# Optimization experiments

Measured on AMD Instinct MI355X. Metric: run time of the kernel, lower is better.

The kernel has to match this reference:

```python
import jax, jax.numpy as jnp
import numpy as np

N = 100000        # number of graph nodes
IN_DIM = 256      # input feature dim
OUT_DIM = 64      # output feature dim
X_NNZ = 1_600_000 # nnz of sparse feature matrix x (avg 16 per node)
A_NNZ = 3_200_000 # nnz of sparse adjacency (avg degree 32)
KEEP_PROB = 0.9   # 1 - dropout


def setup_inputs() -> dict:
    key = jax.random.key(0)
    ks = jax.random.split(key, 8)
    x_vals = jax.random.normal(ks[0], (X_NNZ,), dtype=jnp.float32)
    x_rows = jax.random.randint(ks[1], (X_NNZ,), 0, N, dtype=jnp.int32)
    x_cols = jax.random.randint(ks[2], (X_NNZ,), 0, IN_DIM, dtype=jnp.int32)
    adj_vals = jax.random.uniform(ks[3], (A_NNZ,), dtype=jnp.float32)
    adj_rows = jax.random.randint(ks[4], (A_NNZ,), 0, N, dtype=jnp.int32)
    adj_cols = jax.random.randint(ks[5], (A_NNZ,), 0, N, dtype=jnp.int32)
    # Glorot uniform init, as in weight_variable_glorot
    lim = float(np.sqrt(6.0 / (IN_DIM + OUT_DIM)))
    W = jax.random.uniform(ks[6], (IN_DIM, OUT_DIM), dtype=jnp.float32, minval=-lim, maxval=lim)
    # deterministic dropout retain mask (Bernoulli(keep_prob)), mirrors dropout_sparse
    keep_mask = jax.random.uniform(ks[7], (X_NNZ,)) < KEEP_PROB
    return {
        "x_vals": x_vals, "x_rows": x_rows, "x_cols": x_cols,
        "adj_vals": adj_vals, "adj_rows": adj_rows, "adj_cols": adj_cols,
        "W": W, "keep_mask": keep_mask,
    }


def reference(x_vals, x_rows, x_cols, adj_vals, adj_rows, adj_cols, W, keep_mask):
    # sparse dropout: retain + rescale by 1/keep_prob
    xv = jnp.where(keep_mask, x_vals, jnp.float32(0.0)) * jnp.float32(1.0 / KEEP_PROB)
    # spmm 1: h = x @ W  -> gather W rows by feature col index, scatter-add by node row
    h = jax.ops.segment_sum(xv[:, None] * W[x_cols], x_rows, num_segments=N)  # [N, OUT_DIM]
    # spmm 2: agg = adj @ h -> gather neighbor features, scatter-add by destination node
    agg = jax.ops.segment_sum(adj_vals[:, None] * h[adj_cols], adj_rows, num_segments=N)  # [N, OUT_DIM]
    return jax.nn.relu(agg)
```

## Files before the change

kernel.cpp:

```cpp
#include <hip/hip_runtime.h>
#include <hip/hip_bf16.h>

#define N_NODES 100000
#define IN_DIM 256
#define OUT_DIM 64
#define INV_KEEP 1.1111111111111112f

#define BROWS 256
#define NBUCKET ((N_NODES + BROWS - 1) / BROWS)
#define PBLK 256
#define A_CAP 9728
#define X_CAP 5120

__device__ __forceinline__ int   ldnt (const int* p)   { return __builtin_nontemporal_load(p); }
__device__ __forceinline__ float ldntf(const float* p) { return __builtin_nontemporal_load(p); }

__global__ __launch_bounds__(256) void hist_count_kernel(
    const int* __restrict__ xr, const int* __restrict__ keep,
    const int* __restrict__ ar,
    int* __restrict__ cnt_blk_x, int* __restrict__ cnt_blk_a,
    int x_nnz, int a_nnz)
{
    __shared__ int cnt[NBUCKET];
    const bool isA = blockIdx.x >= PBLK;
    const int ib = isA ? (int)blockIdx.x - PBLK : (int)blockIdx.x;
    const int nnz = isA ? a_nnz : x_nnz;
    const int chunk = (nnz + PBLK - 1) / PBLK;
    const int lo = ib * chunk, hi = min(lo + chunk, nnz);

    for (int k = threadIdx.x; k < NBUCKET; k += 256) cnt[k] = 0;
    __syncthreads();
    if (isA) {
        for (int e = lo + (int)threadIdx.x; e < hi; e += 256)
            atomicAdd(&cnt[ldnt(ar + e) >> 8], 1);
    } else {
        for (int e = lo + (int)threadIdx.x; e < hi; e += 256)
            if (ldnt(keep + e) != 0) atomicAdd(&cnt[ldnt(xr + e) >> 8], 1);
    }
    __syncthreads();
    int* dst = (isA ? cnt_blk_a : cnt_blk_x) + (size_t)ib * NBUCKET;
    for (int k = threadIdx.x; k < NBUCKET; k += 256) dst[k] = cnt[k];
}

__global__ __launch_bounds__(256) void colscan_kernel(
    int* __restrict__ cnt_blk_x, int* __restrict__ cnt_blk_a,
    int* __restrict__ btot_x, int* __restrict__ btot_a)
{
    const bool isA = blockIdx.x >= NBUCKET;
    const int k = isA ? (int)blockIdx.x - NBUCKET : (int)blockIdx.x;
    int* cb = isA ? cnt_blk_a : cnt_blk_x;
    __shared__ int sc[PBLK];
    const int t = threadIdx.x;
    int v = cb[(size_t)t * NBUCKET + k];
    sc[t] = v;
    __syncthreads();
    for (int off = 1; off < PBLK; off <<= 1) {
        int u = (t >= off) ? sc[t - off] : 0;
        __syncthreads();
        sc[t] += u;
        __syncthreads();
    }
    cb[(size_t)t * NBUCKET + k] = sc[t] - v;
    if (t == PBLK - 1) (isA ? btot_a : btot_x)[k] = sc[t];
}

__global__ __launch_bounds__(512) void bucket_scan_kernel(
    const int* __restrict__ btot_x, const int* __restrict__ btot_a,
    int* __restrict__ bstart_x, int* __restrict__ bstart_a)
{
    const int* c = blockIdx.x ? btot_a : btot_x;
    int* bs      = blockIdx.x ? bstart_a : bstart_x;
    __shared__ int sc[512];
    const int t = threadIdx.x;
    sc[t] = (t < NBUCKET) ? c[t] : 0;
    __syncthreads();
    for (int off = 1; off < 512; off <<= 1) {
        int u = (t >= off) ? sc[t - off] : 0;
        __syncthreads();
        sc[t] += u;
        __syncthreads();
    }
    if (t < NBUCKET) bs[t] = (t > 0) ? sc[t - 1] : 0;
    if (t == NBUCKET - 1) bs[NBUCKET] = sc[t];
}

__global__ __launch_bounds__(256) void partition_place_kernel(
    const float* __restrict__ xv, const int* __restrict__ xr,
    const int* __restrict__ xc, const int* __restrict__ keep,
    const float* __restrict__ av, const int* __restrict__ ar,
    const int* __restrict__ ac,
    const int* __restrict__ cnt_blk_x, const int* __restrict__ cnt_blk_a,
    const int* __restrict__ bstart_x, const int* __restrict__ bstart_a,
    float2* __restrict__ xs, float2* __restrict__ as, int x_nnz, int a_nnz)
{
    __shared__ int off_l[NBUCKET];
    const bool isA = blockIdx.x >= PBLK;
    const int ib = isA ? (int)blockIdx.x - PBLK : (int)blockIdx.x;
    const int nnz = isA ? a_nnz : x_nnz;
    const int chunk = (nnz + PBLK - 1) / PBLK;
    const int lo = ib * chunk, hi = min(lo + chunk, nnz);
    const int* cb = (isA ? cnt_blk_a : cnt_blk_x) + (size_t)ib * NBUCKET;
    const int* bs = isA ? bstart_a : bstart_x;
    float2* out   = isA ? as : xs;

    for (int k = threadIdx.x; k < NBUCKET; k += 256) off_l[k] = bs[k] + cb[k];
    __syncthreads();
    if (isA) {
        for (int e = lo + (int)threadIdx.x; e < hi; e += 256) {
            int r = ldnt(ar + e), c = ldnt(ac + e);
            float v = ldntf(av + e);
            int pos = atomicAdd(&off_l[r >> 8], 1);
            out[pos] = make_float2(v, __uint_as_float(((unsigned)c << 8) | (unsigned)(r & (BROWS - 1))));
        }
    } else {
        for (int e = lo + (int)threadIdx.x; e < hi; e += 256) {
            if (ldnt(keep + e) == 0) continue;
            int r = ldnt(xr + e), c = ldnt(xc + e);
            float v = ldntf(xv + e) * INV_KEEP;
            int pos = atomicAdd(&off_l[r >> 8], 1);
            out[pos] = make_float2(v, __uint_as_float(((unsigned)c << 8) | (unsigned)(r & (BROWS - 1))));
        }
    }
}

template <int CAP>
__global__ __launch_bounds__(256) void reorder_kernel(
    const int* __restrict__ bstart, float2* __restrict__ data,
    int* __restrict__ start)
{
    __shared__ float2 recs[CAP];
    __shared__ int rcnt[BROWS];
    __shared__ int sc[BROWS];
    __shared__ int curs[BROWS];
    const int b = blockIdx.x;
    const int brow0 = b * BROWS;
    const int rows_n = min(BROWS, N_NODES - brow0);
    const int base = bstart[b];
    int size = bstart[b + 1] - base;
    if (size > CAP) size = CAP;
    const int t = threadIdx.x;

    rcnt[t] = 0;
    __syncthreads();
    for (int i = t; i < size; i += 256) {
        float2 rec = data[base + i];
        recs[i] = rec;
        atomicAdd(&rcnt[__float_as_uint(rec.y) & (BROWS - 1)], 1);
    }
    __syncthreads();
    sc[t] = rcnt[t];
    __syncthreads();
    for (int off = 1; off < 256; off <<= 1) {
        int v = (t >= off) ? sc[t - off] : 0;
        __syncthreads();
        sc[t] += v;
        __syncthreads();
    }
    int excl = (t > 0) ? sc[t - 1] : 0;
    curs[t] = base + excl;
    if (t < rows_n) start[brow0 + t] = base + excl;
    if (brow0 + rows_n == N_NODES && t == rows_n - 1) start[N_NODES] = base + size;
    __syncthreads();
    for (int i = t; i < size; i += 256) {
        float2 rec = recs[i];
        unsigned u = __float_as_uint(rec.y);
        int pos = atomicAdd(&curs[u & (BROWS - 1)], 1);
        data[pos] = make_float2(rec.x, __int_as_float((int)(u >> 8)));
    }
}


__global__ __launch_bounds__(256) void spmm1_csr_kernel(
    const int* __restrict__ xs_start, const float2* __restrict__ xs,
    const float* __restrict__ W, __hip_bfloat16* __restrict__ h)
{
    const int wave = (int)((blockIdx.x * blockDim.x + threadIdx.x) >> 6);
    const int lane = threadIdx.x & 63;
    if (wave >= N_NODES) return;

    const int s = xs_start[wave];
    const int e = xs_start[wave + 1];
    float acc = 0.0f;
    int j = s;
    for (; j + 4 <= e; j += 4) {
        float2 p0 = xs[j + 0];
        float2 p1 = xs[j + 1];
        float2 p2 = xs[j + 2];
        float2 p3 = xs[j + 3];
        float g0 = W[__float_as_int(p0.y) * OUT_DIM + lane];
        float g1 = W[__float_as_int(p1.y) * OUT_DIM + lane];
        float g2 = W[__float_as_int(p2.y) * OUT_DIM + lane];
        float g3 = W[__float_as_int(p3.y) * OUT_DIM + lane];
        acc += p0.x * g0;
        acc += p1.x * g1;
        acc += p2.x * g2;
        acc += p3.x * g3;
    }
    for (; j < e; ++j) {
        float2 p = xs[j];
        acc += p.x * W[__float_as_int(p.y) * OUT_DIM + lane];
    }
    h[(size_t)wave * OUT_DIM + lane] = __float2bfloat16(acc);
}

__global__ __launch_bounds__(256) void spmm2_csr_kernel(
    const int* __restrict__ as_start, const float2* __restrict__ as,
    const __hip_bfloat16* __restrict__ h, float* __restrict__ out)
{
    const int wave = (int)((blockIdx.x * blockDim.x + threadIdx.x) >> 6);
    const int lane = threadIdx.x & 63;
    if (wave >= N_NODES) return;

    const int s = as_start[wave];
    const int e = as_start[wave + 1];
    float acc = 0.0f;
    int j = s;
    for (; j + 16 <= e; j += 16) {
        float2 q[16];
#pragma unroll
        for (int k = 0; k < 16; ++k) q[k] = as[j + k];
        float g[16];
#pragma unroll
        for (int k = 0; k < 16; ++k)
            g[k] = __bfloat162float(h[(size_t)__float_as_int(q[k].y) * OUT_DIM + lane]);
#pragma unroll
        for (int k = 0; k < 16; ++k) acc += q[k].x * g[k];
    }
    for (; j + 8 <= e; j += 8) {
        float2 q[8];
#pragma unroll
        for (int k = 0; k < 8; ++k) q[k] = as[j + k];
        float g[8];
#pragma unroll
        for (int k = 0; k < 8; ++k)
            g[k] = __bfloat162float(h[(size_t)__float_as_int(q[k].y) * OUT_DIM + lane]);
#pragma unroll
        for (int k = 0; k < 8; ++k) acc += q[k].x * g[k];
    }
    for (; j < e; ++j) {
        float2 p = as[j];
        acc += p.x * __bfloat162float(h[(size_t)__float_as_int(p.y) * OUT_DIM + lane]);
    }
    float r = acc > 0.0f ? acc : 0.0f;
    __builtin_nontemporal_store(r, &out[(size_t)wave * OUT_DIM + lane]);
}


__global__ __launch_bounds__(256) void spmm1_atomic_kernel(
    const float* __restrict__ x_vals, const int* __restrict__ x_rows,
    const int* __restrict__ x_cols, const int* __restrict__ keep,
    const float* __restrict__ W, float* __restrict__ h, int nnz)
{
    const int lane   = threadIdx.x & 63;
    const int group  = (int)((blockIdx.x * blockDim.x + threadIdx.x) >> 6);
    const int stride = (int)((gridDim.x * blockDim.x) >> 6);
    for (int e = group; e < nnz; e += stride) {
        float v = (keep[e] != 0) ? x_vals[e] * INV_KEEP : 0.0f;
        if (v != 0.0f)
            atomicAdd(&h[(size_t)x_rows[e] * OUT_DIM + lane],
                      v * W[x_cols[e] * OUT_DIM + lane]);
    }
}

__global__ __launch_bounds__(256) void spmm2_atomic_kernel(
    const float* __restrict__ adj_vals, const int* __restrict__ adj_rows,
    const int* __restrict__ adj_cols, const float* __restrict__ h,
    float* __restrict__ out, int nnz)
{
    const int lane   = threadIdx.x & 63;
    const int group  = (int)((blockIdx.x * blockDim.x + threadIdx.x) >> 6);
    const int stride = (int)((gridDim.x * blockDim.x) >> 6);
    for (int e = group; e < nnz; e += stride) {
        atomicAdd(&out[(size_t)adj_rows[e] * OUT_DIM + lane],
                  adj_vals[e] * h[(size_t)adj_cols[e] * OUT_DIM + lane]);
    }
}

__global__ __launch_bounds__(256) void relu_kernel(float* __restrict__ out, int n)
{
    int i = (int)(blockIdx.x * blockDim.x + threadIdx.x);
    if (i < n) {
        float v = out[i];
        out[i] = v > 0.0f ? v : 0.0f;
    }
}


extern "C" void kernel_launch(void* const* d_in, const int* in_sizes, int n_in,
                              void* d_out, int out_size, void* d_ws, size_t ws_size,
                              hipStream_t stream)
{
    const float* x_vals   = (const float*)d_in[0];
    const int*   x_rows   = (const int*)d_in[1];
    const int*   x_cols   = (const int*)d_in[2];
    const float* adj_vals = (const float*)d_in[3];
    const int*   adj_rows = (const int*)d_in[4];
    const int*   adj_cols = (const int*)d_in[5];
    const float* W        = (const float*)d_in[6];
    const int*   keep     = (const int*)d_in[7];

    const int x_nnz = in_sizes[0];
    const int a_nnz = in_sizes[3];

    float* out = (float*)d_out;

    char* ws = (char*)d_ws;
    size_t off = 0;
    float2* xs = (float2*)(ws + off);                 off += (size_t)x_nnz * 8;
    float2* as = (float2*)(ws + off);                 off += (size_t)a_nnz * 8;
    __hip_bfloat16* hb = (__hip_bfloat16*)(ws + off); off += (size_t)N_NODES * OUT_DIM * 2;
    int* x_start   = (int*)(ws + off);                off += (size_t)(N_NODES + 1) * 4;
    int* a_start   = (int*)(ws + off);                off += (size_t)(N_NODES + 1) * 4;
    int* cnt_blk_x = (int*)(ws + off);                off += (size_t)PBLK * NBUCKET * 4;
    int* cnt_blk_a = (int*)(ws + off);                off += (size_t)PBLK * NBUCKET * 4;
    int* btot_x    = (int*)(ws + off);                off += (size_t)NBUCKET * 4;
    int* btot_a    = (int*)(ws + off);                off += (size_t)NBUCKET * 4;
    int* bstart_x  = (int*)(ws + off);                off += (size_t)(NBUCKET + 1) * 4;
    int* bstart_a  = (int*)(ws + off);                off += (size_t)(NBUCKET + 1) * 4;
    const size_t needed = off;

    if (ws_size >= needed) {
        hist_count_kernel<<<2 * PBLK, 256, 0, stream>>>(
            x_rows, keep, adj_rows, cnt_blk_x, cnt_blk_a, x_nnz, a_nnz);

        colscan_kernel<<<2 * NBUCKET, 256, 0, stream>>>(
            cnt_blk_x, cnt_blk_a, btot_x, btot_a);

        bucket_scan_kernel<<<2, 512, 0, stream>>>(
            btot_x, btot_a, bstart_x, bstart_a);

        partition_place_kernel<<<2 * PBLK, 256, 0, stream>>>(
            x_vals, x_rows, x_cols, keep, adj_vals, adj_rows, adj_cols,
            cnt_blk_x, cnt_blk_a, bstart_x, bstart_a, xs, as, x_nnz, a_nnz);

        reorder_kernel<X_CAP><<<NBUCKET, 256, 0, stream>>>(bstart_x, xs, x_start);
        reorder_kernel<A_CAP><<<NBUCKET, 256, 0, stream>>>(bstart_a, as, a_start);

        const int blocks = (N_NODES * 64 + 255) / 256;
        spmm1_csr_kernel<<<blocks, 256, 0, stream>>>(x_start, xs, W, hb);
        spmm2_csr_kernel<<<blocks, 256, 0, stream>>>(a_start, as, hb, out);
    } else {
        float* hf = (float*)d_ws;
        hipMemsetAsync(hf, 0, (size_t)N_NODES * OUT_DIM * 4, stream);
        hipMemsetAsync(out, 0, (size_t)out_size * 4, stream);
        spmm1_atomic_kernel<<<4096, 256, 0, stream>>>(x_vals, x_rows, x_cols, keep, W, hf, x_nnz);
        spmm2_atomic_kernel<<<4096, 256, 0, stream>>>(adj_vals, adj_rows, adj_cols, hf, out, a_nnz);
        relu_kernel<<<(out_size + 255) / 256, 256, 0, stream>>>(out, out_size);
    }
}
```

Measured before the change: 301.4 us.

## Fuse x-bucket row reorder into spmm1, computing h directly from shared memory

The separate reorder pass for the feature matrix and the per-row CSR spmm1 kernel are merged into one kernel per 256-row bucket. It sorts the bucket's records by row into shared memory, then each of its 4 waves walks 64 rows and gathers W. This removes one global write and re-read of the x records, the x_start array and a launch. The cost is parallelism: spmm1 now runs on only about 391 blocks with 4 waves each, with serial row loops instead of one wave per row.

```diff
diff --git a/kernel.cpp b/kernel.cpp
--- a/kernel.cpp
+++ b/kernel.cpp
@@ -123,12 +123,80 @@
     }
 }
 
-template <int CAP>
-__global__ __launch_bounds__(256) void reorder_kernel(
+__global__ __launch_bounds__(256) void spmm1_fused_kernel(
+    const int* __restrict__ bstart, const float2* __restrict__ xs,
+    const float* __restrict__ W, __hip_bfloat16* __restrict__ h)
+{
+    __shared__ float2 recs[X_CAP];
+    __shared__ int rcnt[BROWS];
+    __shared__ int rofs[BROWS];
+    __shared__ int curs[BROWS];
+    const int b = blockIdx.x;
+    const int brow0 = b * BROWS;
+    const int rows_n = min(BROWS, N_NODES - brow0);
+    const int base = bstart[b];
+    int size = bstart[b + 1] - base;
+    if (size > X_CAP) size = X_CAP;
+    const int t = threadIdx.x;
+
+    rcnt[t] = 0;
+    __syncthreads();
+    for (int i = t; i < size; i += 256)
+        atomicAdd(&rcnt[__float_as_uint(xs[base + i].y) & (BROWS - 1)], 1);
+    __syncthreads();
+    rofs[t] = rcnt[t];
+    __syncthreads();
+    for (int off = 1; off < 256; off <<= 1) {
+        int v = (t >= off) ? rofs[t - off] : 0;
+        __syncthreads();
+        rofs[t] += v;
+        __syncthreads();
+    }
+    curs[t] = (t > 0) ? rofs[t - 1] : 0;
+    __syncthreads();
+    for (int i = t; i < size; i += 256) {
+        float2 rec = xs[base + i];
+        unsigned u = __float_as_uint(rec.y);
+        int pos = atomicAdd(&curs[u & (BROWS - 1)], 1);
+        recs[pos] = make_float2(rec.x, __int_as_float((int)(u >> 8)));
+    }
+    __syncthreads();
+
+    const int wv = t >> 6, lane = t & 63;
+    for (int rr = 0; rr < 64; ++rr) {
+        const int r = wv * 64 + rr;
+        if (r >= rows_n) break;
+        const int s  = (r > 0) ? rofs[r - 1] : 0;
+        const int e2 = rofs[r];
+        float acc = 0.0f;
+        int j = s;
+        for (; j + 4 <= e2; j += 4) {
+            float2 p0 = recs[j + 0];
+            float2 p1 = recs[j + 1];
+            float2 p2 = recs[j + 2];
+            float2 p3 = recs[j + 3];
+            float g0 = W[__float_as_int(p0.y) * OUT_DIM + lane];
+            float g1 = W[__float_as_int(p1.y) * OUT_DIM + lane];
+            float g2 = W[__float_as_int(p2.y) * OUT_DIM + lane];
+            float g3 = W[__float_as_int(p3.y) * OUT_DIM + lane];
+            acc += p0.x * g0;
+            acc += p1.x * g1;
+            acc += p2.x * g2;
+            acc += p3.x * g3;
+        }
+        for (; j < e2; ++j) {
+            float2 p = recs[j];
+            acc += p.x * W[__float_as_int(p.y) * OUT_DIM + lane];
+        }
+        h[(size_t)(brow0 + r) * OUT_DIM + lane] = __float2bfloat16(acc);
+    }
+}
+
+__global__ __launch_bounds__(256) void reorder_a_kernel(
     const int* __restrict__ bstart, float2* __restrict__ data,
     int* __restrict__ start)
 {
-    __shared__ float2 recs[CAP];
+    __shared__ float2 recs[A_CAP];
     __shared__ int rcnt[BROWS];
     __shared__ int sc[BROWS];
     __shared__ int curs[BROWS];
@@ -137,7 +205,7 @@
     const int rows_n = min(BROWS, N_NODES - brow0);
     const int base = bstart[b];
     int size = bstart[b + 1] - base;
-    if (size > CAP) size = CAP;
+    if (size > A_CAP) size = A_CAP;
     const int t = threadIdx.x;
 
     rcnt[t] = 0;
@@ -167,40 +235,6 @@
         int pos = atomicAdd(&curs[u & (BROWS - 1)], 1);
         data[pos] = make_float2(rec.x, __int_as_float((int)(u >> 8)));
     }
-}
-
-
-__global__ __launch_bounds__(256) void spmm1_csr_kernel(
-    const int* __restrict__ xs_start, const float2* __restrict__ xs,
-    const float* __restrict__ W, __hip_bfloat16* __restrict__ h)
-{
-    const int wave = (int)((blockIdx.x * blockDim.x + threadIdx.x) >> 6);
-    const int lane = threadIdx.x & 63;
-    if (wave >= N_NODES) return;
-
-    const int s = xs_start[wave];
-    const int e = xs_start[wave + 1];
-    float acc = 0.0f;
-    int j = s;
-    for (; j + 4 <= e; j += 4) {
-        float2 p0 = xs[j + 0];
-        float2 p1 = xs[j + 1];
-        float2 p2 = xs[j + 2];
-        float2 p3 = xs[j + 3];
-        float g0 = W[__float_as_int(p0.y) * OUT_DIM + lane];
-        float g1 = W[__float_as_int(p1.y) * OUT_DIM + lane];
-        float g2 = W[__float_as_int(p2.y) * OUT_DIM + lane];
-        float g3 = W[__float_as_int(p3.y) * OUT_DIM + lane];
-        acc += p0.x * g0;
-        acc += p1.x * g1;
-        acc += p2.x * g2;
-        acc += p3.x * g3;
-    }
-    for (; j < e; ++j) {
-        float2 p = xs[j];
-        acc += p.x * W[__float_as_int(p.y) * OUT_DIM + lane];
-    }
-    h[(size_t)wave * OUT_DIM + lane] = __float2bfloat16(acc);
 }
 
 __global__ __launch_bounds__(256) void spmm2_csr_kernel(
@@ -309,7 +343,6 @@
     float2* xs = (float2*)(ws + off);                 off += (size_t)x_nnz * 8;
     float2* as = (float2*)(ws + off);                 off += (size_t)a_nnz * 8;
     __hip_bfloat16* hb = (__hip_bfloat16*)(ws + off); off += (size_t)N_NODES * OUT_DIM * 2;
-    int* x_start   = (int*)(ws + off);                off += (size_t)(N_NODES + 1) * 4;
     int* a_start   = (int*)(ws + off);                off += (size_t)(N_NODES + 1) * 4;
     int* cnt_blk_x = (int*)(ws + off);                off += (size_t)PBLK * NBUCKET * 4;
     int* cnt_blk_a = (int*)(ws + off);                off += (size_t)PBLK * NBUCKET * 4;
@@ -333,11 +366,11 @@
             x_vals, x_rows, x_cols, keep, adj_vals, adj_rows, adj_cols,
             cnt_blk_x, cnt_blk_a, bstart_x, bstart_a, xs, as, x_nnz, a_nnz);
 
-        reorder_kernel<X_CAP><<<NBUCKET, 256, 0, stream>>>(bstart_x, xs, x_start);
-        reorder_kernel<A_CAP><<<NBUCKET, 256, 0, stream>>>(bstart_a, as, a_start);
+        spmm1_fused_kernel<<<NBUCKET, 256, 0, stream>>>(bstart_x, xs, W, hb);
+
+        reorder_a_kernel<<<NBUCKET, 256, 0, stream>>>(bstart_a, as, a_start);
 
         const int blocks = (N_NODES * 64 + 255) / 256;
-        spmm1_csr_kernel<<<blocks, 256, 0, stream>>>(x_start, xs, W, hb);
         spmm2_csr_kernel<<<blocks, 256, 0, stream>>>(a_start, as, hb, out);
     } else {
         float* hf = (float*)d_ws;
```

Result: slower. 312.9 us (+3.8%).
